# Optimization experiments

Measured on AMD Instinct MI355X. Metric: run time of the kernel, lower is better.

## Reference

```python
import jax, jax.numpy as jnp
import numpy as np

N = 20000      # num nodes
E = 320000     # num edges (avg degree 16)
F_IN = 518     # object_feature_dim
D = 128        # node_embedding_dim (= GAT out_channels)
ED = 32        # edge_embedding_dim
R = 26         # num_relations
H = 4          # GAT heads (concat=False -> mean over heads)
HID = 256      # node_encoder hidden


def _gat_layer(x, src, dst, ea, lin, lin_e, att_s, att_d, att_e, bias):
    """PyG GATConv: add_self_loops=True (fill_value='mean'), concat=False, negative_slope=0.2."""
    n = x.shape[0]
    ones = jnp.ones((src.shape[0],), x.dtype)
    cnt = jax.ops.segment_sum(ones, dst, num_segments=n)                    # [N]
    loop_ea = jax.ops.segment_sum(ea, dst, num_segments=n) / jnp.maximum(cnt, 1.0)[:, None]
    idx = jnp.arange(n)
    s = jnp.concatenate([src, idx])
    d = jnp.concatenate([dst, idx])
    ea2 = jnp.concatenate([ea, loop_ea], axis=0)                            # [E+N, ED]
    h = (x @ lin).reshape(n, H, D)                                          # [N,H,D]
    a_s = jnp.einsum('nhd,hd->nh', h, att_s)                                # [N,H]
    a_d = jnp.einsum('nhd,hd->nh', h, att_d)
    e = (ea2 @ lin_e).reshape(-1, H, D)                                     # [E+N,H,D]
    a_e = jnp.einsum('ehd,hd->eh', e, att_e)
    alpha = jax.nn.leaky_relu(a_s[s] + a_d[d] + a_e, 0.2)                   # [E+N,H]
    amax = jax.ops.segment_max(alpha, d, num_segments=n)
    alpha = jnp.exp(alpha - amax[d])
    denom = jax.ops.segment_sum(alpha, d, num_segments=n)
    alpha = alpha / (denom[d] + 1e-16)                                      # segment softmax
    msg = h[s] * alpha[:, :, None]                                          # [E+N,H,D]
    out = jax.ops.segment_sum(msg, d, num_segments=n)                       # [N,H,D]
    return out.mean(axis=1) + bias                                          # concat=False


def setup_inputs() -> dict:
    key = jax.random.key(0)
    ks = jax.random.split(key, 18)
    g = lambda k, shp, s=0.05: jax.random.normal(k, shp, jnp.float32) * s
    return {
        'x': g(ks[0], (N, F_IN), 1.0),
        'edge_index': jax.random.randint(ks[1], (2, E), 0, N),
        'edge_type': jax.random.randint(ks[2], (E,), 0, R),
        'w1': g(ks[3], (F_IN, HID)), 'b1': jnp.zeros((HID,), jnp.float32),
        'w2': g(ks[4], (HID, D)),    'b2': jnp.zeros((D,), jnp.float32),
        'rel_emb': g(ks[5], (R, ED), 1.0),
        'lin1': g(ks[6], (D, H * D)), 'line1': g(ks[7], (ED, H * D)),
        'atts1': g(ks[8], (H, D)), 'attd1': g(ks[9], (H, D)), 'atte1': g(ks[10], (H, D)),
        'bias1': jnp.zeros((D,), jnp.float32),
        'lin2': g(ks[11], (D, H * D)), 'line2': g(ks[12], (ED, H * D)),
        'atts2': g(ks[13], (H, D)), 'attd2': g(ks[14], (H, D)), 'atte2': g(ks[15], (H, D)),
        'bias2': jnp.zeros((D,), jnp.float32),
    }


def reference(x, edge_index, edge_type, w1, b1, w2, b2, rel_emb,
              lin1, line1, atts1, attd1, atte1, bias1,
              lin2, line2, atts2, attd2, atte2, bias2):
    src, dst = edge_index[0], edge_index[1]
    # node encoder (dropout inactive in eval)
    h = jax.nn.relu(x @ w1 + b1) @ w2 + b2                                  # [N,D]
    ea = rel_emb[edge_type]                                                 # [E,ED]
    h = jax.nn.relu(_gat_layer(h, src, dst, ea, lin1, line1, atts1, attd1, atte1, bias1))
    h = jax.nn.relu(_gat_layer(h, src, dst, ea, lin2, line2, atts2, attd2, atte2, bias2))
    return h
```

## Files before the change

### kernel.cpp

```cpp
#include <hip/hip_runtime.h>
#include <math.h>

#define N_NODES 20000
#define MP      20032
#define N_EDGES 320000
#define F_IN    518
#define HIDDEN  256
#define DIM     128
#define NH      4

typedef __attribute__((ext_vector_type(8))) short bf16x8;
typedef __attribute__((ext_vector_type(4))) float f32x4;
typedef unsigned short ushort_t;

__device__ __forceinline__ float lrelu02(float x) { return x > 0.f ? x : 0.2f * x; }

__device__ __forceinline__ void gl_lds16(const void* g, void* l) {
    __builtin_amdgcn_global_load_lds(
        (const __attribute__((address_space(1))) unsigned int*)g,
        (__attribute__((address_space(3))) unsigned int*)l, 16, 0, 0);
}

__device__ __forceinline__ unsigned int hi16(float v) { return __float_as_uint(v) >> 16; }
__device__ __forceinline__ unsigned int lo16(float v) {
    unsigned int h = __float_as_uint(v) & 0xFFFF0000u;
    return __float_as_uint(v - __uint_as_float(h)) >> 16;
}
__device__ __forceinline__ unsigned int rnd16(float v) {
    unsigned int u = __float_as_uint(v);
    return (u + 0x7FFFu + ((u >> 16) & 1u)) >> 16;
}
__device__ __forceinline__ float bfl(unsigned int u) { return __uint_as_float(u << 16); }
__device__ __forceinline__ float bfh(unsigned int u) { return __uint_as_float(u & 0xFFFF0000u); }

__global__ __launch_bounds__(256, 4) void gemm_mfma_v2(
    const ushort_t* __restrict__ Ah, const ushort_t* __restrict__ Al,
    const ushort_t* __restrict__ Bh, const ushort_t* __restrict__ Bl,
    const float* __restrict__ bias,
    int M, int K8, int N, int act,
    float* __restrict__ Cf,
    ushort_t* __restrict__ Ch, ushort_t* __restrict__ Cl,
    ushort_t* __restrict__ Cb,
    ushort_t* __restrict__ Ca)
{
    __shared__ __align__(16) ushort_t lds[12288];
    const int tid = threadIdx.x;
    const int w = tid >> 6, lane = tid & 63;
    const int row0 = blockIdx.y * 64, col0 = blockIdx.x * 128;
    const int nkb = K8 >> 2;
    const int m16 = lane & 15, q = lane >> 4;
    const bool use_al = (Al != nullptr);

    f32x4 acc[4][2] = {};

    for (int kb = 0; kb < nkb; ++kb) {
        const size_t kc = (size_t)(kb * 4 + w);
        const size_t aoff = (kc * MP + row0) * 8 + lane * 8;
        const size_t boff = (kc * N + col0) * 8 + lane * 8;
        gl_lds16(Ah + aoff, &lds[w * 512]);
        if (use_al) gl_lds16(Al + aoff, &lds[2048 + w * 512]);
        gl_lds16(Bh + boff,       &lds[4096 + w * 1024]);
        gl_lds16(Bh + boff + 512, &lds[4096 + w * 1024 + 512]);
        gl_lds16(Bl + boff,       &lds[8192 + w * 1024]);
        gl_lds16(Bl + boff + 512, &lds[8192 + w * 1024 + 512]);
        __syncthreads();

        bf16x8 fah[4], fal[4], fbh[2], fbl[2];
        const int fa = q * 512 + m16 * 8;
        #pragma unroll
        for (int mi = 0; mi < 4; ++mi) {
            fah[mi] = *(const bf16x8*)&lds[fa + mi * 128];
            if (use_al) fal[mi] = *(const bf16x8*)&lds[2048 + fa + mi * 128];
        }
        const int fb = q * 1024 + (w * 32 + m16) * 8;
        #pragma unroll
        for (int ni = 0; ni < 2; ++ni) {
            fbh[ni] = *(const bf16x8*)&lds[4096 + fb + ni * 128];
            fbl[ni] = *(const bf16x8*)&lds[8192 + fb + ni * 128];
        }
        #pragma unroll
        for (int mi = 0; mi < 4; ++mi)
            #pragma unroll
            for (int ni = 0; ni < 2; ++ni) {
                acc[mi][ni] = __builtin_amdgcn_mfma_f32_16x16x32_bf16(fah[mi], fbh[ni], acc[mi][ni], 0, 0, 0);
                acc[mi][ni] = __builtin_amdgcn_mfma_f32_16x16x32_bf16(fah[mi], fbl[ni], acc[mi][ni], 0, 0, 0);
            }
        if (use_al) {
            #pragma unroll
            for (int mi = 0; mi < 4; ++mi)
                #pragma unroll
                for (int ni = 0; ni < 2; ++ni)
                    acc[mi][ni] = __builtin_amdgcn_mfma_f32_16x16x32_bf16(fal[mi], fbh[ni], acc[mi][ni], 0, 0, 0);
        }
        __syncthreads();
    }

    #pragma unroll
    for (int ni = 0; ni < 2; ++ni) {
        const int col = col0 + w * 32 + ni * 16 + m16;
        const float bb = bias ? bias[col] : 0.f;
        #pragma unroll
        for (int mi = 0; mi < 4; ++mi) {
            #pragma unroll
            for (int r = 0; r < 4; ++r) {
                const int row = row0 + mi * 16 + q * 4 + r;
                if (row < M) {
                    float v = acc[mi][ni][r] + bb;
                    if (act) v = fmaxf(v, 0.f);
                    if (Cf) Cf[(size_t)row * N + col] = v;
                    if (Cb) Cb[(size_t)row * N + col] = (ushort_t)rnd16(v);
                    const size_t p = (((size_t)(col >> 3)) * MP + row) * 8 + (col & 7);
                    if (Ch) { Ch[p] = (ushort_t)hi16(v); Cl[p] = (ushort_t)lo16(v); }
                    if (Ca) Ca[p] = (ushort_t)rnd16(v);
                }
            }
        }
    }
}

__global__ __launch_bounds__(256) void conv_a_t_kernel(
    const float* __restrict__ x, ushort_t* __restrict__ xh, ushort_t* __restrict__ xl)
{
    __shared__ float tile[64][68];
    const int tid = threadIdx.x;
    const int r0 = blockIdx.x * 64;
    const int c0 = blockIdx.y * 64;

    #pragma unroll
    for (int it = 0; it < 4; ++it) {
        const int r = (tid >> 4) + it * 16;
        const int c = (tid & 15) * 4;
        const int gr = r0 + r, gc = c0 + c;
        float4 v = {0.f, 0.f, 0.f, 0.f};
        if (gr < N_NODES) {
            if (gc + 3 < F_IN) {
                v = *(const float4*)(x + (size_t)gr * F_IN + gc);
            } else {
                float tmp[4] = {0.f, 0.f, 0.f, 0.f};
                #pragma unroll
                for (int u = 0; u < 4; ++u)
                    if (gc + u < F_IN) tmp[u] = x[(size_t)gr * F_IN + gc + u];
                v.x = tmp[0]; v.y = tmp[1]; v.z = tmp[2]; v.w = tmp[3];
            }
        }
        tile[r][c] = v.x; tile[r][c+1] = v.y; tile[r][c+2] = v.z; tile[r][c+3] = v.w;
    }
    __syncthreads();

    const int k8l = tid >> 5;
    const int k8 = (c0 >> 3) + k8l;
    if (k8 >= 68) return;
    const int rr = (tid & 31) * 2;
    #pragma unroll
    for (int u = 0; u < 2; ++u) {
        const int r = rr + u;
        unsigned int hp[4], lp[4];
        #pragma unroll
        for (int i = 0; i < 4; ++i) {
            const float v0 = tile[r][k8l * 8 + 2 * i];
            const float v1 = tile[r][k8l * 8 + 2 * i + 1];
            hp[i] = (hi16(v1) << 16) | hi16(v0);
            lp[i] = (lo16(v1) << 16) | lo16(v0);
        }
        const size_t p = ((size_t)k8 * MP + r0 + r) * 8;
        *(uint4*)(xh + p) = make_uint4(hp[0], hp[1], hp[2], hp[3]);
        *(uint4*)(xl + p) = make_uint4(lp[0], lp[1], lp[2], lp[3]);
    }
}

#define W1_T (68 * 256 * 8)
#define W2_T (32 * 128 * 8)
#define L_T  (16 * 512 * 8)
__global__ __launch_bounds__(256) void conv_w_all_kernel(
    const float* __restrict__ w1, const float* __restrict__ w2,
    const float* __restrict__ l0, const float* __restrict__ l1,
    ushort_t* __restrict__ w1h, ushort_t* __restrict__ w1l,
    ushort_t* __restrict__ w2h, ushort_t* __restrict__ w2l,
    ushort_t* __restrict__ l0h, ushort_t* __restrict__ l0l,
    ushort_t* __restrict__ l1h, ushort_t* __restrict__ l1l)
{
    int idx = blockIdx.x * 256 + threadIdx.x;
    const float* w; ushort_t *bh, *bl; int K, N, local;
    if (idx < W1_T) { w = w1; bh = w1h; bl = w1l; K = F_IN; N = HIDDEN; local = idx; }
    else if (idx < W1_T + W2_T) { w = w2; bh = w2h; bl = w2l; K = HIDDEN; N = DIM; local = idx - W1_T; }
    else if (idx < W1_T + W2_T + L_T) { w = l0; bh = l0h; bl = l0l; K = DIM; N = 512; local = idx - W1_T - W2_T; }
    else if (idx < W1_T + W2_T + 2 * L_T) { w = l1; bh = l1h; bl = l1l; K = DIM; N = 512; local = idx - W1_T - W2_T - L_T; }
    else return;
    const int j = local & 7;
    const int rem = local >> 3;
    const int n = rem % N;
    const int k = (rem / N) * 8 + j;
    const float v = (k < K) ? w[(size_t)k * N + n] : 0.f;
    bh[local] = (ushort_t)hi16(v);
    bl[local] = (ushort_t)lo16(v);
}

__global__ __launch_bounds__(256) void wa2_kernel(
    const float* __restrict__ lin0, const float* __restrict__ lin1,
    const float* __restrict__ atts0, const float* __restrict__ attd0,
    const float* __restrict__ atts1, const float* __restrict__ attd1,
    float* __restrict__ wa_s0, float* __restrict__ wa_d0,
    float* __restrict__ wa_s1, float* __restrict__ wa_d1)
{
    const int wrk = blockIdx.x * 256 + threadIdx.x;
    if (wrk >= 2048) return;
    const int L = wrk >> 10;
    const int sd = (wrk >> 9) & 1;
    const int p = wrk & 511;
    const int h = p >> 7, d = p & 127;
    const float* lin = L ? lin1 : lin0;
    const float* av = L ? (sd ? attd1 : atts1) : (sd ? attd0 : atts0);
    float* out = L ? (sd ? wa_d1 : wa_s1) : (sd ? wa_d0 : wa_s0);
    const float* lp = lin + (size_t)d * (NH * DIM) + h * DIM;
    const float* ap = av + h * DIM;
    float acc = 0.f;
    #pragma unroll 8
    for (int i = 0; i < DIM; ++i) acc += lp[i] * ap[i];
    out[h * DIM + d] = acc;
}

__global__ __launch_bounds__(256) void as_ad_kernel(
    const float* __restrict__ xb, const float* __restrict__ wa_s,
    const float* __restrict__ wa_d, float* __restrict__ a_s, float* __restrict__ a_d)
{
    const int gw = blockIdx.x * 4 + (threadIdx.x >> 6);
    const int lane = threadIdx.x & 63;
    if (gw >= N_NODES * NH) return;
    const int n = gw >> 2, h = gw & 3;
    const float* hp = xb + (size_t)n * DIM;
    float2 hv = *(const float2*)(hp + lane * 2);
    float2 sv = *(const float2*)(wa_s + h * DIM + lane * 2);
    float2 dv = *(const float2*)(wa_d + h * DIM + lane * 2);
    float s = hv.x * sv.x + hv.y * sv.y;
    float d = hv.x * dv.x + hv.y * dv.y;
    #pragma unroll
    for (int off = 32; off > 0; off >>= 1) {
        s += __shfl_down(s, off);
        d += __shfl_down(d, off);
    }
    if (lane == 0) { a_s[n * 4 + h] = s; a_d[n * 4 + h] = d; }
}

__global__ __launch_bounds__(128) void rel_table2_kernel(
    const float* __restrict__ rel_emb,
    const float* __restrict__ line0, const float* __restrict__ atte0,
    const float* __restrict__ line1, const float* __restrict__ atte1,
    float* __restrict__ table)
{
    __shared__ float we[32][NH];
    const int L = blockIdx.x;
    const float* line = L ? line1 : line0;
    const float* atte = L ? atte1 : atte0;
    float* tab = table + L * 128;
    const int tid = threadIdx.x;
    const int k = tid >> 2, h = tid & 3;
    float acc = 0.f;
    for (int d = 0; d < DIM; ++d)
        acc += line[(size_t)k * (NH * DIM) + h * DIM + d] * atte[h * DIM + d];
    we[k][h] = acc;
    __syncthreads();
    if (tid < 26 * NH) {
        int r = tid >> 2, hh = tid & 3;
        float t = 0.f;
        for (int kk = 0; kk < 32; ++kk) t += rel_emb[r * 32 + kk] * we[kk][hh];
        tab[r * 4 + hh] = t;
    }
}

__global__ __launch_bounds__(256) void hist_kernel(
    const int* __restrict__ dst, int* __restrict__ cnt)
{
    const int e = blockIdx.x * blockDim.x + threadIdx.x;
    if (e >= N_EDGES) return;
    atomicAdd(&cnt[dst[e]], 1);
}

__global__ __launch_bounds__(1024) void scan_kernel(
    const int* __restrict__ cnt, int* __restrict__ ptr, int* __restrict__ ptr_copy)
{
    __shared__ int tsum[1024];
    const int tid = threadIdx.x;
    const int CH = 20;
    const int base = tid * CH;
    int s = 0;
    #pragma unroll
    for (int i = 0; i < CH; ++i) {
        int idx = base + i;
        if (idx < N_NODES) s += cnt[idx];
    }
    tsum[tid] = s;
    __syncthreads();
    for (int off = 1; off < 1024; off <<= 1) {
        int v = (tid >= off) ? tsum[tid - off] : 0;
        __syncthreads();
        tsum[tid] += v;
        __syncthreads();
    }
    int run = (tid == 0) ? 0 : tsum[tid - 1];
    #pragma unroll
    for (int i = 0; i < CH; ++i) {
        int idx = base + i;
        if (idx < N_NODES) {
            ptr[idx] = run;
            ptr_copy[idx] = run;
            run += cnt[idx];
        }
    }
    if (tid == 0) ptr[N_NODES] = N_EDGES;
}

__global__ __launch_bounds__(256) void scatter_kernel(
    const int* __restrict__ src, const int* __restrict__ dst, const int* __restrict__ etype,
    int* __restrict__ ptr_copy, int2* __restrict__ se, int* __restrict__ pose)
{
    const int e = blockIdx.x * blockDim.x + threadIdx.x;
    if (e >= N_EDGES) return;
    const int d = dst[e];
    const int pos = atomicAdd(&ptr_copy[d], 1);
    se[pos] = make_int2(src[e], etype[e]);
    pose[e] = pos;
}

#define EP_EBLK (N_EDGES / 256)
__global__ __launch_bounds__(256) void edge_self_p_kernel(
    const int* __restrict__ src, const int* __restrict__ dst, const int* __restrict__ etype,
    const int* __restrict__ pose, const int* __restrict__ ptr, const int2* __restrict__ se,
    const float* __restrict__ a_s, const float* __restrict__ a_d,
    const float* __restrict__ table, float* __restrict__ p4, float* __restrict__ sp)
{
    const int b = blockIdx.x;
    if (b < EP_EBLK) {
        const int e = b * 256 + threadIdx.x;
        const int s = src[e], d = dst[e], et = etype[e];
        const float4 as = *(const float4*)(a_s + s * 4);
        const float4 ad = *(const float4*)(a_d + d * 4);
        const float4 t  = *(const float4*)(table + et * 4);
        float4 o;
        o.x = __expf(lrelu02(as.x + ad.x + t.x));
        o.y = __expf(lrelu02(as.y + ad.y + t.y));
        o.z = __expf(lrelu02(as.z + ad.z + t.z));
        o.w = __expf(lrelu02(as.w + ad.w + t.w));
        *(float4*)(p4 + (size_t)pose[e] * 4) = o;
    } else {
        const int n = (b - EP_EBLK) * 256 + threadIdx.x;
        if (n >= N_NODES) return;
        const int beg = ptr[n], end = ptr[n + 1];
        float t0 = 0.f, t1 = 0.f, t2 = 0.f, t3 = 0.f;
        for (int j = beg; j < end; ++j) {
            const float4 t = *(const float4*)(table + se[j].y * 4);
            t0 += t.x; t1 += t.y; t2 += t.z; t3 += t.w;
        }
        const float inv = 1.0f / fmaxf((float)(end - beg), 1.0f);
        const float4 as = *(const float4*)(a_s + n * 4);
        const float4 ad = *(const float4*)(a_d + n * 4);
        float4 o;
        o.x = __expf(lrelu02(as.x + ad.x + t0 * inv));
        o.y = __expf(lrelu02(as.y + ad.y + t1 * inv));
        o.z = __expf(lrelu02(as.z + ad.z + t2 * inv));
        o.w = __expf(lrelu02(as.w + ad.w + t3 * inv));
        *(float4*)(sp + n * 4) = o;
    }
}

__device__ __forceinline__ void acc8(float acc[8], float p, const uint4 g)
{
    acc[0] += p * bfl(g.x); acc[1] += p * bfh(g.x);
    acc[2] += p * bfl(g.y); acc[3] += p * bfh(g.y);
    acc[4] += p * bfl(g.z); acc[5] += p * bfh(g.z);
    acc[6] += p * bfl(g.w); acc[7] += p * bfh(g.w);
}

__device__ __forceinline__ void agg_loop(
    int beg, int end, int n, int head, int cbase,
    const int2* __restrict__ se, const float* __restrict__ p4,
    const float* __restrict__ sp, const ushort_t* __restrict__ hb,
    float acc[8], float& dh)
{
    const uint4 gs = *(const uint4*)(hb + (size_t)n * 512 + cbase);
    const float ps = sp[n * 4 + head];

    int j = beg;
    for (; j + 4 <= end; j += 4) {
        const int2 e0 = se[j],     e1 = se[j + 1];
        const int2 e2 = se[j + 2], e3 = se[j + 3];
        const float* pj = p4 + ((size_t)j * 4 + head);
        const float p0 = pj[0], p1 = pj[4], p2 = pj[8], p3 = pj[12];
        const uint4 g0 = *(const uint4*)(hb + (size_t)e0.x * 512 + cbase);
        const uint4 g1 = *(const uint4*)(hb + (size_t)e1.x * 512 + cbase);
        const uint4 g2 = *(const uint4*)(hb + (size_t)e2.x * 512 + cbase);
        const uint4 g3 = *(const uint4*)(hb + (size_t)e3.x * 512 + cbase);
        dh += (p0 + p1) + (p2 + p3);
        acc8(acc, p0, g0); acc8(acc, p1, g1);
        acc8(acc, p2, g2); acc8(acc, p3, g3);
    }
    for (; j + 2 <= end; j += 2) {
        const int2 e0 = se[j], e1 = se[j + 1];
        const float* pj = p4 + ((size_t)j * 4 + head);
        const float p0 = pj[0], p1 = pj[4];
        const uint4 g0 = *(const uint4*)(hb + (size_t)e0.x * 512 + cbase);
        const uint4 g1 = *(const uint4*)(hb + (size_t)e1.x * 512 + cbase);
        dh += p0 + p1;
        acc8(acc, p0, g0); acc8(acc, p1, g1);
    }
    if (j < end) {
        const int2 e0 = se[j];
        const float p0 = p4[(size_t)j * 4 + head];
        const uint4 g0 = *(const uint4*)(hb + (size_t)e0.x * 512 + cbase);
        dh += p0;
        acc8(acc, p0, g0);
    }
    dh += ps;
    acc8(acc, ps, gs);
}

__global__ __launch_bounds__(256) void node_agg_f_kernel(
    const int* __restrict__ ptr, const int2* __restrict__ se,
    const float* __restrict__ p4, const float* __restrict__ sp,
    const ushort_t* __restrict__ hb,
    const float* __restrict__ bias, ushort_t* __restrict__ oa,
    const float* __restrict__ wa_s2, const float* __restrict__ wa_d2,
    float* __restrict__ a_s2, float* __restrict__ a_d2)
{
    const int n = blockIdx.x * 4 + (threadIdx.x >> 6);
    const int lane = threadIdx.x & 63;
    if (n >= N_NODES) return;
    const int beg = ptr[n], end = ptr[n + 1];
    const int head = lane >> 4;
    const int cbase = lane * 8;

    float acc[8] = {};
    float dh = 0.f;
    agg_loop(beg, end, n, head, cbase, se, p4, sp, hb, acc, dh);

    const float ih = 0.25f / (dh + 1e-16f);
    float t[8];
    #pragma unroll
    for (int k = 0; k < 8; ++k) {
        t[k] = acc[k] * ih;
        t[k] += __shfl_xor(t[k], 16);
        t[k] += __shfl_xor(t[k], 32);
    }
    if (lane < 16) {
        const float4 b0 = *(const float4*)(bias + cbase);
        const float4 b1 = *(const float4*)(bias + cbase + 4);
        float o[8];
        o[0] = fmaxf(t[0] + b0.x, 0.f); o[1] = fmaxf(t[1] + b0.y, 0.f);
        o[2] = fmaxf(t[2] + b0.z, 0.f); o[3] = fmaxf(t[3] + b0.w, 0.f);
        o[4] = fmaxf(t[4] + b1.x, 0.f); o[5] = fmaxf(t[5] + b1.y, 0.f);
        o[6] = fmaxf(t[6] + b1.z, 0.f); o[7] = fmaxf(t[7] + b1.w, 0.f);
        unsigned int up[4];
        #pragma unroll
        for (int i = 0; i < 4; ++i)
            up[i] = (rnd16(o[2*i+1]) << 16) | rnd16(o[2*i]);
        *(uint4*)(oa + ((size_t)lane * MP + n) * 8) = make_uint4(up[0], up[1], up[2], up[3]);
        float pss[4] = {0,0,0,0}, pdd[4] = {0,0,0,0};
        #pragma unroll
        for (int h = 0; h < NH; ++h) {
            const float* ws = wa_s2 + h * DIM + cbase;
            const float* wd = wa_d2 + h * DIM + cbase;
            #pragma unroll
            for (int i = 0; i < 8; ++i) {
                pss[h] += o[i] * ws[i];
                pdd[h] += o[i] * wd[i];
            }
        }
        #pragma unroll
        for (int m = 1; m < 16; m <<= 1) {
            #pragma unroll
            for (int h = 0; h < NH; ++h) {
                pss[h] += __shfl_xor(pss[h], m);
                pdd[h] += __shfl_xor(pdd[h], m);
            }
        }
        if (lane == 0) {
            float4 vs = {pss[0], pss[1], pss[2], pss[3]};
            float4 vd = {pdd[0], pdd[1], pdd[2], pdd[3]};
            *(float4*)(a_s2 + n * 4) = vs;
            *(float4*)(a_d2 + n * 4) = vd;
        }
    }
}

__global__ __launch_bounds__(256) void node_agg_s_kernel(
    const int* __restrict__ ptr, const int2* __restrict__ se,
    const float* __restrict__ p4, const float* __restrict__ sp,
    const ushort_t* __restrict__ hb,
    const float* __restrict__ bias, float* __restrict__ outf)
{
    const int n = blockIdx.x * 4 + (threadIdx.x >> 6);
    const int lane = threadIdx.x & 63;
    if (n >= N_NODES) return;
    const int beg = ptr[n], end = ptr[n + 1];
    const int head = lane >> 4;
    const int cbase = lane * 8;

    float acc[8] = {};
    float dh = 0.f;
    agg_loop(beg, end, n, head, cbase, se, p4, sp, hb, acc, dh);

    const float ih = 0.25f / (dh + 1e-16f);
    float t[8];
    #pragma unroll
    for (int k = 0; k < 8; ++k) {
        t[k] = acc[k] * ih;
        t[k] += __shfl_xor(t[k], 16);
        t[k] += __shfl_xor(t[k], 32);
    }
    if (lane < 16) {
        const float4 b0 = *(const float4*)(bias + cbase);
        const float4 b1 = *(const float4*)(bias + cbase + 4);
        float4 v0, v1;
        v0.x = fmaxf(t[0] + b0.x, 0.f); v0.y = fmaxf(t[1] + b0.y, 0.f);
        v0.z = fmaxf(t[2] + b0.z, 0.f); v0.w = fmaxf(t[3] + b0.w, 0.f);
        v1.x = fmaxf(t[4] + b1.x, 0.f); v1.y = fmaxf(t[5] + b1.y, 0.f);
        v1.z = fmaxf(t[6] + b1.z, 0.f); v1.w = fmaxf(t[7] + b1.w, 0.f);
        *(float4*)(outf + (size_t)n * DIM + cbase) = v0;
        *(float4*)(outf + (size_t)n * DIM + cbase + 4) = v1;
    }
}

extern "C" void kernel_launch(void* const* d_in, const int* in_sizes, int n_in,
                              void* d_out, int out_size, void* d_ws, size_t ws_size,
                              hipStream_t stream)
{
    const float* x       = (const float*)d_in[0];
    const int*   eidx    = (const int*)d_in[1];
    const int*   etype   = (const int*)d_in[2];
    const float* w1      = (const float*)d_in[3];
    const float* b1      = (const float*)d_in[4];
    const float* w2      = (const float*)d_in[5];
    const float* b2      = (const float*)d_in[6];
    const float* rel_emb = (const float*)d_in[7];
    const float* lin[2]  = {(const float*)d_in[8],  (const float*)d_in[14]};
    const float* line[2] = {(const float*)d_in[9],  (const float*)d_in[15]};
    const float* atts[2] = {(const float*)d_in[10], (const float*)d_in[16]};
    const float* attd[2] = {(const float*)d_in[11], (const float*)d_in[17]};
    const float* atte[2] = {(const float*)d_in[12], (const float*)d_in[18]};
    const float* bias[2] = {(const float*)d_in[13], (const float*)d_in[19]};
    const int* src = eidx;
    const int* dst = eidx + N_EDGES;

    char* base = (char*)d_ws;
    size_t off = 0;
    auto alloc = [&](size_t bytes) -> void* {
        void* p = base + off;
        off = (off + bytes + 255) & ~(size_t)255;
        return p;
    };
    ushort_t* xh  = (ushort_t*)alloc((size_t)68 * MP * 8 * 2);
    ushort_t* xl  = (ushort_t*)alloc((size_t)68 * MP * 8 * 2);
    ushort_t* h1h = (ushort_t*)alloc((size_t)32 * MP * 8 * 2);
    ushort_t* h1l = (ushort_t*)alloc((size_t)32 * MP * 8 * 2);
    ushort_t* x0a = (ushort_t*)alloc((size_t)16 * MP * 8 * 2);
    void* reg1    = alloc((size_t)16 * MP * 8 * 4);
    ushort_t* w1h = (ushort_t*)alloc(W1_T * 2);
    ushort_t* w1l = (ushort_t*)alloc(W1_T * 2);
    ushort_t* w2h = (ushort_t*)alloc(W2_T * 2);
    ushort_t* w2l = (ushort_t*)alloc(W2_T * 2);
    ushort_t* l0h = (ushort_t*)alloc(L_T * 2);
    ushort_t* l0l = (ushort_t*)alloc(L_T * 2);
    ushort_t* l1h = (ushort_t*)alloc(L_T * 2);
    ushort_t* l1l = (ushort_t*)alloc(L_T * 2);
    float* a_s0  = (float*)alloc(N_NODES * 4 * 4);
    float* a_d0  = (float*)alloc(N_NODES * 4 * 4);
    float* a_s1  = (float*)alloc(N_NODES * 4 * 4);
    float* a_d1  = (float*)alloc(N_NODES * 4 * 4);
    float* table = (float*)alloc(2 * 128 * 4);
    float* wa_s0 = (float*)alloc(512 * 4);
    float* wa_d0 = (float*)alloc(512 * 4);
    float* wa_s1 = (float*)alloc(512 * 4);
    float* wa_d1 = (float*)alloc(512 * 4);
    int*  cnt_i  = (int*)alloc(N_NODES * 4);
    int*  ptr    = (int*)alloc((N_NODES + 4) * 4);
    int*  ptrc   = (int*)alloc(N_NODES * 4);
    int2* se     = (int2*)alloc((size_t)N_EDGES * 8);
    int*  pose   = (int*)alloc((size_t)N_EDGES * 4);
    float* p4    = (float*)alloc((size_t)N_EDGES * 4 * 4);
    float* sp    = (float*)alloc((size_t)N_NODES * 4 * 4);

    ushort_t* hb = xh;
    float* xbuf0 = (float*)reg1;
    ushort_t* x1a = (ushort_t*)reg1;

    const int mtiles = MP / 64;
    const int ep_grid = EP_EBLK + (N_NODES + 255) / 256;

    conv_a_t_kernel<<<dim3(MP / 64, 9), 256, 0, stream>>>(x, xh, xl);
    conv_w_all_kernel<<<(W1_T + W2_T + 2 * L_T + 255) / 256, 256, 0, stream>>>(
        w1, w2, lin[0], lin[1], w1h, w1l, w2h, w2l, l0h, l0l, l1h, l1l);
    wa2_kernel<<<8, 256, 0, stream>>>(lin[0], lin[1], atts[0], attd[0], atts[1], attd[1],
                                      wa_s0, wa_d0, wa_s1, wa_d1);
    rel_table2_kernel<<<2, 128, 0, stream>>>(rel_emb, line[0], atte[0], line[1], atte[1], table);

    hipMemsetAsync(cnt_i, 0, N_NODES * sizeof(int), stream);
    hist_kernel<<<(N_EDGES + 255) / 256, 256, 0, stream>>>(dst, cnt_i);
    scan_kernel<<<1, 1024, 0, stream>>>(cnt_i, ptr, ptrc);
    scatter_kernel<<<(N_EDGES + 255) / 256, 256, 0, stream>>>(src, dst, etype, ptrc, se, pose);

    gemm_mfma_v2<<<dim3(HIDDEN / 128, mtiles), 256, 0, stream>>>(
        xh, xl, w1h, w1l, b1, N_NODES, 68, HIDDEN, 1, nullptr, h1h, h1l, nullptr, nullptr);
    gemm_mfma_v2<<<dim3(DIM / 128, mtiles), 256, 0, stream>>>(
        h1h, h1l, w2h, w2l, b2, N_NODES, 32, DIM, 0, xbuf0, nullptr, nullptr, nullptr, x0a);

    gemm_mfma_v2<<<dim3((NH * DIM) / 128, mtiles), 256, 0, stream>>>(
        x0a, nullptr, l0h, l0l, nullptr, N_NODES, 16, NH * DIM, 0, nullptr, nullptr, nullptr, hb, nullptr);
    as_ad_kernel<<<N_NODES, 256, 0, stream>>>(xbuf0, wa_s0, wa_d0, a_s0, a_d0);
    edge_self_p_kernel<<<ep_grid, 256, 0, stream>>>(
        src, dst, etype, pose, ptr, se, a_s0, a_d0, table, p4, sp);
    node_agg_f_kernel<<<(N_NODES + 3) / 4, 256, 0, stream>>>(
        ptr, se, p4, sp, hb, bias[0], x1a,
        wa_s1, wa_d1, a_s1, a_d1);

    gemm_mfma_v2<<<dim3((NH * DIM) / 128, mtiles), 256, 0, stream>>>(
        x1a, nullptr, l1h, l1l, nullptr, N_NODES, 16, NH * DIM, 0, nullptr, nullptr, nullptr, hb, nullptr);
    edge_self_p_kernel<<<ep_grid, 256, 0, stream>>>(
        src, dst, etype, pose, ptr, se, a_s1, a_d1, table + 128, p4, sp);
    node_agg_s_kernel<<<(N_NODES + 3) / 4, 256, 0, stream>>>(
        ptr, se, p4, sp, hb, bias[1], (float*)d_out);
}
```

Measured before the change: 436.3 us.

## Compute edge logits in CSR order and fuse self-loop logit into aggregation

The edge-logit kernel now walks edges in CSR order using a stored destination array, so p4 is written contiguously instead of being scattered through a position map. The self-loop logit, previously computed by separate threads in the edge kernel, is now computed inside the aggregation loop by accumulating table entries for each head. This drops the sp buffer and the serial per-node loop in the edge kernel. The cost is extra table lookups in the aggregation inner loop and a per-lane exp.

New measurement: 419.0 us. 4.0% less time.

```diff
diff --git a/kernel.cpp b/kernel.cpp
--- a/kernel.cpp
+++ b/kernel.cpp
@@ -311,55 +311,41 @@
 
 __global__ __launch_bounds__(256) void scatter_kernel(
     const int* __restrict__ src, const int* __restrict__ dst, const int* __restrict__ etype,
-    int* __restrict__ ptr_copy, int2* __restrict__ se, int* __restrict__ pose)
+    int* __restrict__ ptr_copy, int2* __restrict__ se, int* __restrict__ dcsr)
 {
     const int e = blockIdx.x * blockDim.x + threadIdx.x;
     if (e >= N_EDGES) return;
     const int d = dst[e];
     const int pos = atomicAdd(&ptr_copy[d], 1);
     se[pos] = make_int2(src[e], etype[e]);
-    pose[e] = pos;
-}
-
-#define EP_EBLK (N_EDGES / 256)
-__global__ __launch_bounds__(256) void edge_self_p_kernel(
-    const int* __restrict__ src, const int* __restrict__ dst, const int* __restrict__ etype,
-    const int* __restrict__ pose, const int* __restrict__ ptr, const int2* __restrict__ se,
+    dcsr[pos] = d;
+}
+
+__global__ __launch_bounds__(256) void edge_p_kernel(
+    const int2* __restrict__ se, const int* __restrict__ dcsr,
     const float* __restrict__ a_s, const float* __restrict__ a_d,
-    const float* __restrict__ table, float* __restrict__ p4, float* __restrict__ sp)
-{
-    const int b = blockIdx.x;
-    if (b < EP_EBLK) {
-        const int e = b * 256 + threadIdx.x;
-        const int s = src[e], d = dst[e], et = etype[e];
-        const float4 as = *(const float4*)(a_s + s * 4);
-        const float4 ad = *(const float4*)(a_d + d * 4);
-        const float4 t  = *(const float4*)(table + et * 4);
-        float4 o;
-        o.x = __expf(lrelu02(as.x + ad.x + t.x));
-        o.y = __expf(lrelu02(as.y + ad.y + t.y));
-        o.z = __expf(lrelu02(as.z + ad.z + t.z));
-        o.w = __expf(lrelu02(as.w + ad.w + t.w));
-        *(float4*)(p4 + (size_t)pose[e] * 4) = o;
-    } else {
-        const int n = (b - EP_EBLK) * 256 + threadIdx.x;
-        if (n >= N_NODES) return;
-        const int beg = ptr[n], end = ptr[n + 1];
-        float t0 = 0.f, t1 = 0.f, t2 = 0.f, t3 = 0.f;
-        for (int j = beg; j < end; ++j) {
-            const float4 t = *(const float4*)(table + se[j].y * 4);
-            t0 += t.x; t1 += t.y; t2 += t.z; t3 += t.w;
-        }
-        const float inv = 1.0f / fmaxf((float)(end - beg), 1.0f);
-        const float4 as = *(const float4*)(a_s + n * 4);
-        const float4 ad = *(const float4*)(a_d + n * 4);
-        float4 o;
-        o.x = __expf(lrelu02(as.x + ad.x + t0 * inv));
-        o.y = __expf(lrelu02(as.y + ad.y + t1 * inv));
-        o.z = __expf(lrelu02(as.z + ad.z + t2 * inv));
-        o.w = __expf(lrelu02(as.w + ad.w + t3 * inv));
-        *(float4*)(sp + n * 4) = o;
-    }
+    const float* __restrict__ table, float* __restrict__ p4)
+{
+    const int j0 = (blockIdx.x * 256 + threadIdx.x) * 2;
+    const int2 eA = se[j0], eB = se[j0 + 1];
+    const int dA = dcsr[j0], dB = dcsr[j0 + 1];
+    const float4 asA = *(const float4*)(a_s + eA.x * 4);
+    const float4 asB = *(const float4*)(a_s + eB.x * 4);
+    const float4 adA = *(const float4*)(a_d + dA * 4);
+    const float4 adB = *(const float4*)(a_d + dB * 4);
+    const float4 tA  = *(const float4*)(table + eA.y * 4);
+    const float4 tB  = *(const float4*)(table + eB.y * 4);
+    float4 oA, oB;
+    oA.x = __expf(lrelu02(asA.x + adA.x + tA.x));
+    oA.y = __expf(lrelu02(asA.y + adA.y + tA.y));
+    oA.z = __expf(lrelu02(asA.z + adA.z + tA.z));
+    oA.w = __expf(lrelu02(asA.w + adA.w + tA.w));
+    oB.x = __expf(lrelu02(asB.x + adB.x + tB.x));
+    oB.y = __expf(lrelu02(asB.y + adB.y + tB.y));
+    oB.z = __expf(lrelu02(asB.z + adB.z + tB.z));
+    oB.w = __expf(lrelu02(asB.w + adB.w + tB.w));
+    *(float4*)(p4 + (size_t)j0 * 4)     = oA;
+    *(float4*)(p4 + (size_t)j0 * 4 + 4) = oB;
 }
 
 __device__ __forceinline__ void acc8(float acc[8], float p, const uint4 g)
@@ -373,12 +359,12 @@
 __device__ __forceinline__ void agg_loop(
     int beg, int end, int n, int head, int cbase,
     const int2* __restrict__ se, const float* __restrict__ p4,
-    const float* __restrict__ sp, const ushort_t* __restrict__ hb,
-    float acc[8], float& dh)
+    const float* __restrict__ table, const float* __restrict__ a_s, float adh,
+    const ushort_t* __restrict__ hb, float acc[8], float& dh)
 {
     const uint4 gs = *(const uint4*)(hb + (size_t)n * 512 + cbase);
-    const float ps = sp[n * 4 + head];
-
+
+    float eh = 0.f;
     int j = beg;
     for (; j + 4 <= end; j += 4) {
         const int2 e0 = se[j],     e1 = se[j + 1];
@@ -389,6 +375,8 @@
         const uint4 g1 = *(const uint4*)(hb + (size_t)e1.x * 512 + cbase);
         const uint4 g2 = *(const uint4*)(hb + (size_t)e2.x * 512 + cbase);
         const uint4 g3 = *(const uint4*)(hb + (size_t)e3.x * 512 + cbase);
+        eh += (table[e0.y * 4 + head] + table[e1.y * 4 + head])
+            + (table[e2.y * 4 + head] + table[e3.y * 4 + head]);
         dh += (p0 + p1) + (p2 + p3);
         acc8(acc, p0, g0); acc8(acc, p1, g1);
         acc8(acc, p2, g2); acc8(acc, p3, g3);
@@ -399,6 +387,7 @@
         const float p0 = pj[0], p1 = pj[4];
         const uint4 g0 = *(const uint4*)(hb + (size_t)e0.x * 512 + cbase);
         const uint4 g1 = *(const uint4*)(hb + (size_t)e1.x * 512 + cbase);
+        eh += table[e0.y * 4 + head] + table[e1.y * 4 + head];
         dh += p0 + p1;
         acc8(acc, p0, g0); acc8(acc, p1, g1);
     }
@@ -406,16 +395,20 @@
         const int2 e0 = se[j];
         const float p0 = p4[(size_t)j * 4 + head];
         const uint4 g0 = *(const uint4*)(hb + (size_t)e0.x * 512 + cbase);
+        eh += table[e0.y * 4 + head];
         dh += p0;
         acc8(acc, p0, g0);
     }
+    const float inv = 1.0f / fmaxf((float)(end - beg), 1.0f);
+    const float ps = __expf(lrelu02(a_s[n * 4 + head] + adh + eh * inv));
     dh += ps;
     acc8(acc, ps, gs);
 }
 
 __global__ __launch_bounds__(256) void node_agg_f_kernel(
     const int* __restrict__ ptr, const int2* __restrict__ se,
-    const float* __restrict__ p4, const float* __restrict__ sp,
+    const float* __restrict__ p4, const float* __restrict__ table,
+    const float* __restrict__ a_s, const float* __restrict__ a_d,
     const ushort_t* __restrict__ hb,
     const float* __restrict__ bias, ushort_t* __restrict__ oa,
     const float* __restrict__ wa_s2, const float* __restrict__ wa_d2,
@@ -427,10 +420,11 @@
     const int beg = ptr[n], end = ptr[n + 1];
     const int head = lane >> 4;
     const int cbase = lane * 8;
+    const float adh = a_d[n * 4 + head];
 
     float acc[8] = {};
     float dh = 0.f;
-    agg_loop(beg, end, n, head, cbase, se, p4, sp, hb, acc, dh);
+    agg_loop(beg, end, n, head, cbase, se, p4, table, a_s, adh, hb, acc, dh);
 
     const float ih = 0.25f / (dh + 1e-16f);
     float t[8];
@@ -483,7 +477,8 @@
 
 __global__ __launch_bounds__(256) void node_agg_s_kernel(
     const int* __restrict__ ptr, const int2* __restrict__ se,
-    const float* __restrict__ p4, const float* __restrict__ sp,
+    const float* __restrict__ p4, const float* __restrict__ table,
+    const float* __restrict__ a_s, const float* __restrict__ a_d,
     const ushort_t* __restrict__ hb,
     const float* __restrict__ bias, float* __restrict__ outf)
 {
@@ -493,10 +488,11 @@
     const int beg = ptr[n], end = ptr[n + 1];
     const int head = lane >> 4;
     const int cbase = lane * 8;
+    const float adh = a_d[n * 4 + head];
 
     float acc[8] = {};
     float dh = 0.f;
-    agg_loop(beg, end, n, head, cbase, se, p4, sp, hb, acc, dh);
+    agg_loop(beg, end, n, head, cbase, se, p4, table, a_s, adh, hb, acc, dh);
 
     const float ih = 0.25f / (dh + 1e-16f);
     float t[8];
@@ -574,16 +570,15 @@
     int*  ptr    = (int*)alloc((N_NODES + 4) * 4);
     int*  ptrc   = (int*)alloc(N_NODES * 4);
     int2* se     = (int2*)alloc((size_t)N_EDGES * 8);
-    int*  pose   = (int*)alloc((size_t)N_EDGES * 4);
+    int*  dcsr   = (int*)alloc((size_t)N_EDGES * 4);
     float* p4    = (float*)alloc((size_t)N_EDGES * 4 * 4);
-    float* sp    = (float*)alloc((size_t)N_NODES * 4 * 4);
 
     ushort_t* hb = xh;
     float* xbuf0 = (float*)reg1;
     ushort_t* x1a = (ushort_t*)reg1;
 
     const int mtiles = MP / 64;
-    const int ep_grid = EP_EBLK + (N_NODES + 255) / 256;
+    const int ep_grid = N_EDGES / 512;
 
     conv_a_t_kernel<<<dim3(MP / 64, 9), 256, 0, stream>>>(x, xh, xl);
     conv_w_all_kernel<<<(W1_T + W2_T + 2 * L_T + 255) / 256, 256, 0, stream>>>(
@@ -595,7 +590,7 @@
     hipMemsetAsync(cnt_i, 0, N_NODES * sizeof(int), stream);
     hist_kernel<<<(N_EDGES + 255) / 256, 256, 0, stream>>>(dst, cnt_i);
     scan_kernel<<<1, 1024, 0, stream>>>(cnt_i, ptr, ptrc);
-    scatter_kernel<<<(N_EDGES + 255) / 256, 256, 0, stream>>>(src, dst, etype, ptrc, se, pose);
+    scatter_kernel<<<(N_EDGES + 255) / 256, 256, 0, stream>>>(src, dst, etype, ptrc, se, dcsr);
 
     gemm_mfma_v2<<<dim3(HIDDEN / 128, mtiles), 256, 0, stream>>>(
         xh, xl, w1h, w1l, b1, N_NODES, 68, HIDDEN, 1, nullptr, h1h, h1l, nullptr, nullptr);
@@ -605,16 +600,14 @@
     gemm_mfma_v2<<<dim3((NH * DIM) / 128, mtiles), 256, 0, stream>>>(
         x0a, nullptr, l0h, l0l, nullptr, N_NODES, 16, NH * DIM, 0, nullptr, nullptr, nullptr, hb, nullptr);
     as_ad_kernel<<<N_NODES, 256, 0, stream>>>(xbuf0, wa_s0, wa_d0, a_s0, a_d0);
-    edge_self_p_kernel<<<ep_grid, 256, 0, stream>>>(
-        src, dst, etype, pose, ptr, se, a_s0, a_d0, table, p4, sp);
+    edge_p_kernel<<<ep_grid, 256, 0, stream>>>(se, dcsr, a_s0, a_d0, table, p4);
     node_agg_f_kernel<<<(N_NODES + 3) / 4, 256, 0, stream>>>(
-        ptr, se, p4, sp, hb, bias[0], x1a,
+        ptr, se, p4, table, a_s0, a_d0, hb, bias[0], x1a,
         wa_s1, wa_d1, a_s1, a_d1);
 
     gemm_mfma_v2<<<dim3((NH * DIM) / 128, mtiles), 256, 0, stream>>>(
         x1a, nullptr, l1h, l1l, nullptr, N_NODES, 16, NH * DIM, 0, nullptr, nullptr, nullptr, hb, nullptr);
-    edge_self_p_kernel<<<ep_grid, 256, 0, stream>>>(
-        src, dst, etype, pose, ptr, se, a_s1, a_d1, table + 128, p4, sp);
+    edge_p_kernel<<<ep_grid, 256, 0, stream>>>(se, dcsr, a_s1, a_d1, table + 128, p4);
     node_agg_s_kernel<<<(N_NODES + 3) / 4, 256, 0, stream>>>(
-        ptr, se, p4, sp, hb, bias[1], (float*)d_out);
-}
+        ptr, se, p4, table + 128, a_s1, a_d1, hb, bias[1], (float*)d_out);
+}
```
